# Kernel tuning notes

Hardware: AMD Instinct MI355X
Metric: run time of the kernel (lower is better)

The kernel has to match this reference:

```python
import jax, jax.numpy as jnp
import numpy as np
from jax import lax

T = 16        # in_length
E = 32        # input_embedding_size_d
H = 64        # encoder_size
NG = 32       # vehicles per scene group
G = 1024      # number of scene groups
N = G * NG    # total vehicles
C = 3         # class_num

leaky = lambda x: jax.nn.leaky_relu(x, 0.1)

def _gru_final(x_seq, Wih, Whh, bih, bhh):
    # x_seq: (T, N, E). PyTorch GRU gate order: r, z, n. Returns final hidden (N, H).
    def step(h, x):
        gx = x @ Wih.T + bih
        gh = h @ Whh.T + bhh
        xr, xz, xn = jnp.split(gx, 3, axis=-1)
        hr, hz, hn = jnp.split(gh, 3, axis=-1)
        r = jax.nn.sigmoid(xr + hr)
        z = jax.nn.sigmoid(xz + hz)
        ng = jnp.tanh(xn + r * hn)
        return (1.0 - z) * ng + z * h, None
    h0 = jnp.zeros((x_seq.shape[1], Whh.shape[1]), x_seq.dtype)
    hT, _ = lax.scan(step, h0, x_seq)
    return hT

def setup_inputs() -> dict:
    key = jax.random.key(0)
    ks = jax.random.split(key, 24)
    def rn(k, shape, fan):
        return jax.random.normal(k, shape, jnp.float32) * np.float32(1.0 / np.sqrt(fan))
    inp = {}
    inp["scene"] = jax.random.normal(ks[0], (N, 2 * T), jnp.float32)
    inp["condition"] = jax.random.randint(ks[1], (N,), 0, C, jnp.int32)
    inp["hero_pos_index"] = jax.random.randint(ks[2], (G,), 0, N, jnp.int32)
    inp["nbrs_pos_index"] = jax.random.randint(ks[3], (N,), 0, N, jnp.int32)
    inp["index_div"] = jnp.arange(N, dtype=jnp.int32).reshape(G, NG)
    # ip_emb_d: Linear(2, E)
    inp["W_emb"] = rn(ks[4], (2, E), 2)
    inp["b_emb"] = jnp.zeros((E,), jnp.float32)
    # forward / backward GRUs (weight_ih: (3H,E), weight_hh: (3H,H))
    inp["Wih_f"] = rn(ks[5], (3 * H, E), E); inp["Whh_f"] = rn(ks[6], (3 * H, H), H)
    inp["bih_f"] = jnp.zeros((3 * H,), jnp.float32); inp["bhh_f"] = jnp.zeros((3 * H,), jnp.float32)
    inp["Wih_b"] = rn(ks[7], (3 * H, E), E); inp["Whh_b"] = rn(ks[8], (3 * H, H), H)
    inp["bih_b"] = jnp.zeros((3 * H,), jnp.float32); inp["bhh_b"] = jnp.zeros((3 * H,), jnp.float32)
    # mlp: Linear(H, H//2)
    inp["Wm"] = rn(ks[9], (H, H // 2), H); inp["bm"] = jnp.zeros((H // 2,), jnp.float32)
    # spatial_mlp: Linear(2T, H) -> Linear(H, H//2)
    inp["Ws1"] = rn(ks[10], (2 * T, H), 2 * T); inp["bs1"] = jnp.zeros((H,), jnp.float32)
    inp["Ws2"] = rn(ks[11], (H, H // 2), H); inp["bs2"] = jnp.zeros((H // 2,), jnp.float32)
    # op_d: Linear(H, H//4) -> Linear(H//4, C)
    inp["Wo1"] = rn(ks[12], (H, H // 4), H); inp["bo1"] = jnp.zeros((H // 4,), jnp.float32)
    inp["Wo2"] = rn(ks[13], (H // 4, C), H // 4); inp["bo2"] = jnp.zeros((C,), jnp.float32)
    return inp

def reference(scene, condition, hero_pos_index, nbrs_pos_index, index_div,
              W_emb, b_emb, Wih_f, Whh_f, bih_f, bhh_f, Wih_b, Whh_b, bih_b, bhh_b,
              Wm, bm, Ws1, bs1, Ws2, bs2, Wo1, bo1, Wo2, bo2):
    n_total = scene.shape[0]
    # scene.view(-1,2,T).permute(2,0,1) -> (T, N, 2)
    scene_t = scene.reshape(n_total, 2, T).transpose(2, 0, 1)
    emb = leaky(scene_t @ W_emb + b_emb)                 # (T, N, E)
    h_f = _gru_final(emb, Wih_f, Whh_f, bih_f, bhh_f)    # (N, H)
    h_b = _gru_final(emb[::-1], Wih_b, Whh_b, bih_b, bhh_b)
    seq_enc = leaky(((h_f + h_b) * 0.5) @ Wm + bm)       # (N, H//2)
    # pairwise relative features within each group: rel[g, j, i] = x_i - x_j
    feat_g = scene[index_div]                            # (G, n, 2T); row layout == permute(1,2,0).view(-1,2T)
    rel = feat_g[:, None, :, :] - feat_g[:, :, None, :]  # (G, n, n, 2T)
    enc = leaky(leaky(rel @ Ws1 + bs1) @ Ws2 + bs2)      # (G, n, n, H//2)
    # diagonal pairs (i==j) are dropped in the original; subtract mlp(0) then divide by n-1
    zero_enc = leaky(leaky(bs1) @ Ws2 + bs2)             # (H//2,)
    n_grp = index_div.shape[1]
    pooled = (enc.sum(axis=2) - zero_enc) / (n_grp - 1)  # (G, n, H//2)
    pooled = pooled.reshape(n_total, -1)                 # group-concat order == vehicle order (arange groups)
    full_enc = jnp.concatenate([seq_enc, pooled], axis=1)  # (N, H)
    x_logit = leaky(full_enc @ Wo1 + bo1) @ Wo2 + bo2      # (N, C)
    return x_logit, full_enc
```

## Files before the change

### kernel.cpp

```cpp
#include <hip/hip_runtime.h>
#include <hip/hip_bf16.h>

#define TT 16
#define EE 32
#define HH 64
#define NGRP 32
#define CC 3

typedef __attribute__((ext_vector_type(8))) short short8;
typedef __attribute__((ext_vector_type(4))) float floatx4;

#define MFMA16(a, b, c) __builtin_amdgcn_mfma_f32_16x16x32_bf16((a), (b), (c), 0, 0, 0)

#define RLN2 1.4426950408889634f

__device__ __forceinline__ float leakyf(float x) { return fmaxf(x, 0.1f * x); }
__device__ __forceinline__ short f2bf(float x) {
    unsigned u = __float_as_uint(x);
    return (short)((u + 0x7FFFu + ((u >> 16) & 1u)) >> 16);
}
__device__ __forceinline__ short f2bf_h(float x) {
    return (short)((__float_as_uint(x) + 0x8000u) >> 16);
}
__device__ __forceinline__ float bf2f(short s) {
    return __uint_as_float(((unsigned)(unsigned short)s) << 16);
}
__device__ __forceinline__ short8 ld8bfs(const float* __restrict__ p, float s) {
    const float4 a = *(const float4*)p;
    const float4 b = *(const float4*)(p + 4);
    short8 v;
    v[0] = f2bf(a.x * s); v[1] = f2bf(a.y * s); v[2] = f2bf(a.z * s); v[3] = f2bf(a.w * s);
    v[4] = f2bf(b.x * s); v[5] = f2bf(b.y * s); v[6] = f2bf(b.z * s); v[7] = f2bf(b.w * s);
    return v;
}

__global__ __launch_bounds__(512, 6) void fused_kernel(
    const float* __restrict__ scene, const int* __restrict__ index_div,
    const float* __restrict__ W_emb, const float* __restrict__ b_emb,
    const float* __restrict__ Wih_f, const float* __restrict__ Whh_f,
    const float* __restrict__ bih_f, const float* __restrict__ bhh_f,
    const float* __restrict__ Wih_b, const float* __restrict__ Whh_b,
    const float* __restrict__ bih_b, const float* __restrict__ bhh_b,
    const float* __restrict__ Wm, const float* __restrict__ bm,
    const float* __restrict__ Ws1, const float* __restrict__ bs1,
    const float* __restrict__ Ws2, const float* __restrict__ bs2,
    const float* __restrict__ Wo1, const float* __restrict__ bo1,
    const float* __restrict__ Wo2, const float* __restrict__ bo2,
    float* __restrict__ full_enc, float* __restrict__ out)
{
    __shared__ __align__(16) union SmemU {
        struct {
            short Xall[16 * 2 * 64 * 8];
            short Hf[2 * 2 * 2 * 64 * 8];
        } g;
        struct {
            float su[NGRP][68];
            float fe[NGRP][68];
            float swo1[1024];
            float szero[32];
            float sscene2[32][33];
        } s;
    } sm;

    const int g    = blockIdx.x;
    const int tid  = threadIdx.x;
    const int lane = tid & 63;
    const int w    = __builtin_amdgcn_readfirstlane(tid >> 6);
    const int dir  = w >> 2;
    const int wd   = w & 3;
    const int cc   = lane & 15;
    const int quad = lane >> 4;
    const int j    = wd * 16 + cc;
    const int ks_w = j >> 5;
    const int qa_w = (j >> 3) & 3;
    const int ii_w = j & 7;
    const int rlane = (lane & 48) | ((lane & 3) << 2) | ((lane >> 2) & 3);

    {
        float* sc0 = (float*)sm.g.Hf;
        #pragma unroll
        for (int rep = 0; rep < 2; ++rep) {
            const int idx = tid + rep * 512;
            const int v = idx >> 5, c = idx & 31;
            const int n = index_div[g * NGRP + v];
            sc0[c * 33 + v] = scene[n * 32 + c];
        }
    }

    const float* Wih = dir ? Wih_b : Wih_f;
    const float* Whh = dir ? Whh_b : Whh_f;
    const float* bih = dir ? bih_b : bih_f;
    const float* bhh = dir ? bhh_b : bhh_f;
    const int k0 = quad * 8;
    const float SRZ = -RLN2, SN = 2.0f * RLN2;
    const short8 Br0  = ld8bfs(Whh + (j      ) * 64 + k0,      SRZ);
    const short8 Br1  = ld8bfs(Whh + (j      ) * 64 + 32 + k0, SRZ);
    const short8 Br2  = ld8bfs(Wih + (j      ) * 32 + k0,      SRZ);
    const short8 Bz0  = ld8bfs(Whh + (j +  64) * 64 + k0,      SRZ);
    const short8 Bz1  = ld8bfs(Whh + (j +  64) * 64 + 32 + k0, SRZ);
    const short8 Bz2  = ld8bfs(Wih + (j +  64) * 32 + k0,      SRZ);
    const short8 Bhn0 = ld8bfs(Whh + (j + 128) * 64 + k0,      SN);
    const short8 Bhn1 = ld8bfs(Whh + (j + 128) * 64 + 32 + k0, SN);
    const short8 Bxn  = ld8bfs(Wih + (j + 128) * 32 + k0,      SN);
    const float vb_r  = SRZ * (bih[j] + bhh[j]);
    const float vb_z  = SRZ * (bih[j + 64] + bhh[j + 64]);
    const float vb_xn = SN * bih[j + 128];
    const float vb_hn = SN * bhh[j + 128];

    __syncthreads();

    {
        const float* sc0 = (const float*)sm.g.Hf;
        const int t   = tid >> 5;
        const int veh = tid & 31;
        const float xs = sc0[t * 33 + veh];
        const float ys = sc0[(16 + t) * 33 + veh];
        const int mt = veh >> 4;
        const int m  = veh & 15;
        #pragma unroll
        for (int q = 0; q < 4; ++q) {
            short8 v;
            #pragma unroll
            for (int i2 = 0; i2 < 8; ++i2) {
                const int e = q * 8 + i2;
                v[i2] = f2bf(leakyf(fmaf(xs, W_emb[e], fmaf(ys, W_emb[EE + e], b_emb[e]))));
            }
            *(short8*)&sm.g.Xall[(((t * 2 + mt) * 64) + q * 16 + m) * 8] = v;
        }
    }
    __syncthreads();
    {
        const short8 z8 = {0, 0, 0, 0, 0, 0, 0, 0};
        *(short8*)&sm.g.Hf[tid * 8] = z8;
    }

    float h_reg[8];
    #pragma unroll
    for (int i = 0; i < 8; ++i) h_reg[i] = 0.0f;

    const int hf_dir = dir * 2048;
    __syncthreads();

    #pragma unroll 1
    for (int s = 0; s < TT; ++s) {
        const int t  = dir ? (TT - 1 - s) : s;
        const short* HfD = &sm.g.Hf[hf_dir];
        #pragma unroll
        for (int mt = 0; mt < 2; ++mt) {
            const short8 Ah0 = *(const short8*)&HfD[((0 * 2 + mt) * 64 + rlane) * 8];
            const short8 Ah1 = *(const short8*)&HfD[((1 * 2 + mt) * 64 + rlane) * 8];
            const short8 Axx = *(const short8*)&sm.g.Xall[((t * 2 + mt) * 64 + lane) * 8];
            const floatx4 z4 = {0.f, 0.f, 0.f, 0.f};

            const floatx4 ar = MFMA16(Axx, Br2, MFMA16(Ah1, Br1, MFMA16(Ah0, Br0, z4)));
            float rr[4];
            #pragma unroll
            for (int r = 0; r < 4; ++r)
                rr[r] = __builtin_amdgcn_rcpf(1.0f + __builtin_amdgcn_exp2f(ar[r] + vb_r));
            __builtin_amdgcn_sched_barrier(0);

            const floatx4 ahn = MFMA16(Ah1, Bhn1, MFMA16(Ah0, Bhn0, z4));
            const floatx4 axn = MFMA16(Axx, Bxn, z4);
            float ng[4];
            #pragma unroll
            for (int r = 0; r < 4; ++r) {
                const float y = fmaf(rr[r], ahn[r] + vb_hn, axn[r] + vb_xn);
                ng[r] = fmaf(-2.0f,
                             __builtin_amdgcn_rcpf(__builtin_amdgcn_exp2f(y) + 1.0f),
                             1.0f);
            }
            __builtin_amdgcn_sched_barrier(0);

            const floatx4 az = MFMA16(Axx, Bz2, MFMA16(Ah1, Bz1, MFMA16(Ah0, Bz0, z4)));
            #pragma unroll
            for (int r = 0; r < 4; ++r) {
                const float zz = __builtin_amdgcn_rcpf(1.0f + __builtin_amdgcn_exp2f(az[r] + vb_z));
                const float h0 = h_reg[mt * 4 + r];
                h_reg[mt * 4 + r] = fmaf(zz, h0 - ng[r], ng[r]);
            }
        }
        __syncthreads();
        short* HfW = &sm.g.Hf[hf_dir];
        #pragma unroll
        for (int mt = 0; mt < 2; ++mt) {
            #pragma unroll
            for (int r = 0; r < 4; ++r) {
                const int slot = qa_w * 16 + r * 4 + quad;
                HfW[((ks_w * 2 + mt) * 64 + slot) * 8 + ii_w] = f2bf_h(h_reg[mt * 4 + r]);
            }
        }
        __syncthreads();
    }

    #pragma unroll
    for (int rep = 0; rep < 2; ++rep) {
        const int idx = tid + rep * 512;
        const int v = idx >> 5, c = idx & 31;
        const int n = index_div[g * NGRP + v];
        sm.s.sscene2[c][v] = scene[n * 32 + c];
    }
    __syncthreads();

    if (w < 4) {
        const int nt   = w >> 1;
        const int mt_e = w & 1;
        const int n_col = nt * 16 + cc;
        short8 Bm0, Bm1;
        #pragma unroll
        for (int i = 0; i < 8; ++i) {
            Bm0[i] = f2bf(Wm[(     quad * 8 + i) * 32 + n_col]);
            Bm1[i] = f2bf(Wm[(32 + quad * 8 + i) * 32 + n_col]);
        }
        short8 A0, A1;
        #pragma unroll
        for (int ks = 0; ks < 2; ++ks) {
            const short8 F = *(const short8*)&sm.g.Hf[0    + ((ks * 2 + mt_e) * 64 + rlane) * 8];
            const short8 B = *(const short8*)&sm.g.Hf[2048 + ((ks * 2 + mt_e) * 64 + rlane) * 8];
            #pragma unroll
            for (int i = 0; i < 8; ++i) {
                const short v = f2bf(0.5f * (bf2f(F[i]) + bf2f(B[i])));
                if (ks == 0) A0[i] = v; else A1[i] = v;
            }
        }
        const floatx4 z4 = {0.f, 0.f, 0.f, 0.f};
        const floatx4 acc = MFMA16(A1, Bm1, MFMA16(A0, Bm0, z4));
        const float bmn = bm[n_col];
        #pragma unroll
        for (int r = 0; r < 4; ++r) {
            const int veh = mt_e * 16 + quad * 4 + r;
            const float sv = leakyf(acc[r] + bmn);
            const int n = index_div[g * NGRP + veh];
            full_enc[n * HH + n_col] = sv;
            sm.s.fe[veh][n_col] = sv;
        }
    } else {
        const int l  = tid & 255;
        const int v  = l >> 3;
        const int d0 = (l & 7) * 8;
        float acc[8];
        #pragma unroll
        for (int i = 0; i < 8; ++i) acc[i] = 0.0f;
        #pragma unroll
        for (int e = 0; e < EE; ++e) {
            const float f = sm.s.sscene2[e][v];
            const float4 w0 = *(const float4*)&Ws1[e * 64 + d0];
            const float4 w1 = *(const float4*)&Ws1[e * 64 + d0 + 4];
            acc[0] = fmaf(f, w0.x, acc[0]); acc[1] = fmaf(f, w0.y, acc[1]);
            acc[2] = fmaf(f, w0.z, acc[2]); acc[3] = fmaf(f, w0.w, acc[3]);
            acc[4] = fmaf(f, w1.x, acc[4]); acc[5] = fmaf(f, w1.y, acc[5]);
            acc[6] = fmaf(f, w1.z, acc[6]); acc[7] = fmaf(f, w1.w, acc[7]);
        }
        #pragma unroll
        for (int i = 0; i < 8; ++i) sm.s.su[v][d0 + i] = acc[i];
        *(float4*)&sm.s.swo1[l * 4] = *(const float4*)&Wo1[l * 4];
        if (l < 32) {
            float zs = bs2[l];
            #pragma unroll
            for (int d = 0; d < HH; ++d) zs = fmaf(leakyf(bs1[d]), Ws2[d * 32 + l], zs);
            sm.s.szero[l] = leakyf(zs);
        }
    }

    short8 Bw00, Bw01, Bw10, Bw11;
    #pragma unroll
    for (int i = 0; i < 8; ++i) {
        Bw00[i] = f2bf(Ws2[(     quad * 8 + i) * 32 + cc]);
        Bw01[i] = f2bf(Ws2[(32 + quad * 8 + i) * 32 + cc]);
        Bw10[i] = f2bf(Ws2[(     quad * 8 + i) * 32 + 16 + cc]);
        Bw11[i] = f2bf(Ws2[(32 + quad * 8 + i) * 32 + 16 + cc]);
    }
    float bsq0[8], bsq1[8];
    #pragma unroll
    for (int i = 0; i < 8; ++i) {
        bsq0[i] = bs1[quad * 8 + i];
        bsq1[i] = bs1[32 + quad * 8 + i];
    }
    const float bs2c0 = bs2[cc], bs2c1 = bs2[16 + cc];
    __syncthreads();

    #pragma unroll 2
    for (int jj = 0; jj < 4; ++jj) {
        const int jrow = w * 4 + jj;
        float vj0[8], vj1[8];
        #pragma unroll
        for (int i = 0; i < 8; ++i) {
            vj0[i] = sm.s.su[jrow][quad * 8 + i] - bsq0[i];
            vj1[i] = sm.s.su[jrow][32 + quad * 8 + i] - bsq1[i];
        }
        float acc0 = 0.0f, acc1 = 0.0f;
        #pragma unroll
        for (int it = 0; it < 2; ++it) {
            const int irow = it * 16 + cc;
            const float4 p0 = *(const float4*)&sm.s.su[irow][quad * 8];
            const float4 p1 = *(const float4*)&sm.s.su[irow][quad * 8 + 4];
            const float4 p2 = *(const float4*)&sm.s.su[irow][32 + quad * 8];
            const float4 p3 = *(const float4*)&sm.s.su[irow][32 + quad * 8 + 4];
            short8 A0, A1;
            A0[0] = f2bf(leakyf(p0.x - vj0[0])); A0[1] = f2bf(leakyf(p0.y - vj0[1]));
            A0[2] = f2bf(leakyf(p0.z - vj0[2])); A0[3] = f2bf(leakyf(p0.w - vj0[3]));
            A0[4] = f2bf(leakyf(p1.x - vj0[4])); A0[5] = f2bf(leakyf(p1.y - vj0[5]));
            A0[6] = f2bf(leakyf(p1.z - vj0[6])); A0[7] = f2bf(leakyf(p1.w - vj0[7]));
            A1[0] = f2bf(leakyf(p2.x - vj1[0])); A1[1] = f2bf(leakyf(p2.y - vj1[1]));
            A1[2] = f2bf(leakyf(p2.z - vj1[2])); A1[3] = f2bf(leakyf(p2.w - vj1[3]));
            A1[4] = f2bf(leakyf(p3.x - vj1[4])); A1[5] = f2bf(leakyf(p3.y - vj1[5]));
            A1[6] = f2bf(leakyf(p3.z - vj1[6])); A1[7] = f2bf(leakyf(p3.w - vj1[7]));
            const floatx4 z4 = {0.f, 0.f, 0.f, 0.f};
            const floatx4 D0 = MFMA16(A1, Bw01, MFMA16(A0, Bw00, z4));
            const floatx4 D1 = MFMA16(A1, Bw11, MFMA16(A0, Bw10, z4));
            #pragma unroll
            for (int r = 0; r < 4; ++r) {
                acc0 += leakyf(D0[r] + bs2c0);
                acc1 += leakyf(D1[r] + bs2c1);
            }
        }
        acc0 += __shfl_xor(acc0, 16, 64); acc0 += __shfl_xor(acc0, 32, 64);
        acc1 += __shfl_xor(acc1, 16, 64); acc1 += __shfl_xor(acc1, 32, 64);
        const int n = index_div[g * NGRP + jrow];
        if (quad == 0) {
            const float pv = (acc0 - sm.s.szero[cc]) * (1.0f / 31.0f);
            full_enc[n * HH + 32 + cc] = pv;
            sm.s.fe[jrow][32 + cc] = pv;
        } else if (quad == 1) {
            const float pv = (acc1 - sm.s.szero[16 + cc]) * (1.0f / 31.0f);
            full_enc[n * HH + 48 + cc] = pv;
            sm.s.fe[jrow][48 + cc] = pv;
        }
    }
    __syncthreads();

    {
        const int veh = tid >> 4;
        const int p   = tid & 15;
        float a = bo1[p];
        #pragma unroll
        for (int k = 0; k < HH; ++k)
            a = fmaf(sm.s.fe[veh][k], sm.s.swo1[k * 16 + p], a);
        a = leakyf(a);
        float l0 = a * Wo2[p * 3 + 0];
        float l1 = a * Wo2[p * 3 + 1];
        float l2 = a * Wo2[p * 3 + 2];
        #pragma unroll
        for (int off = 1; off < 16; off <<= 1) {
            l0 += __shfl_xor(l0, off, 64);
            l1 += __shfl_xor(l1, off, 64);
            l2 += __shfl_xor(l2, off, 64);
        }
        if (p == 0) {
            const int n = index_div[g * NGRP + veh];
            out[n * 3 + 0] = l0 + bo2[0];
            out[n * 3 + 1] = l1 + bo2[1];
            out[n * 3 + 2] = l2 + bo2[2];
        }
    }
}

extern "C" void kernel_launch(void* const* d_in, const int* in_sizes, int n_in,
                              void* d_out, int out_size, void* d_ws, size_t ws_size,
                              hipStream_t stream) {
    const float* scene     = (const float*)d_in[0];
    const int*   index_div = (const int*)d_in[4];
    const float* W_emb = (const float*)d_in[5];
    const float* b_emb = (const float*)d_in[6];
    const float* Wih_f = (const float*)d_in[7];
    const float* Whh_f = (const float*)d_in[8];
    const float* bih_f = (const float*)d_in[9];
    const float* bhh_f = (const float*)d_in[10];
    const float* Wih_b = (const float*)d_in[11];
    const float* Whh_b = (const float*)d_in[12];
    const float* bih_b = (const float*)d_in[13];
    const float* bhh_b = (const float*)d_in[14];
    const float* Wm  = (const float*)d_in[15];
    const float* bm  = (const float*)d_in[16];
    const float* Ws1 = (const float*)d_in[17];
    const float* bs1 = (const float*)d_in[18];
    const float* Ws2 = (const float*)d_in[19];
    const float* bs2 = (const float*)d_in[20];
    const float* Wo1 = (const float*)d_in[21];
    const float* bo1 = (const float*)d_in[22];
    const float* Wo2 = (const float*)d_in[23];
    const float* bo2 = (const float*)d_in[24];

    const int N = in_sizes[0] / (2 * TT);
    const int G = in_sizes[4] / NGRP;

    float* out      = (float*)d_out;
    float* full_enc = out + (size_t)N * CC;

    fused_kernel<<<dim3(G), dim3(512), 0, stream>>>(
        scene, index_div, W_emb, b_emb, Wih_f, Whh_f, bih_f, bhh_f,
        Wih_b, Whh_b, bih_b, bhh_b, Wm, bm, Ws1, bs1, Ws2, bs2,
        Wo1, bo1, Wo2, bo2, full_enc, out);
}
```

Measured before the change: 213.8 us.

## Pre-pack GRU weights to bf16 workspace and reload per step to cut registers

A one-block prep kernel converts and scales the GRU weight fragments to bf16 once and stores them in a workspace. The fused kernel stops holding all nine weight fragments in registers. It reloads them from the workspace inside each timestep, and the gate loops are restructured so the r, n and z phases each cover both row tiles. This lowers register pressure to improve occupancy or scheduling, at the cost of extra global/L2 loads per step and an additional kernel launch.

```diff
diff --git a/kernel.cpp b/kernel.cpp
--- a/kernel.cpp
+++ b/kernel.cpp
@@ -34,18 +34,49 @@
     return v;
 }
 
+__global__ __launch_bounds__(512) void prep_kernel(
+    const float* __restrict__ Wih_f, const float* __restrict__ Whh_f,
+    const float* __restrict__ Wih_b, const float* __restrict__ Whh_b,
+    short* __restrict__ wsf)
+{
+    const int tid  = threadIdx.x;
+    const int widx = tid >> 6;
+    const int lane = tid & 63;
+    const int dir  = widx >> 2;
+    const int wd   = widx & 3;
+    const int cc   = lane & 15;
+    const int quad = lane >> 4;
+    const int j    = wd * 16 + cc;
+    const int k0   = quad * 8;
+    const float* Wih = dir ? Wih_b : Wih_f;
+    const float* Whh = dir ? Whh_b : Whh_f;
+    const float SRZ = -RLN2, SN = 2.0f * RLN2;
+    short8 f[9];
+    f[0] = ld8bfs(Whh + (j      ) * 64 + k0,      SRZ);
+    f[1] = ld8bfs(Whh + (j      ) * 64 + 32 + k0, SRZ);
+    f[2] = ld8bfs(Wih + (j      ) * 32 + k0,      SRZ);
+    f[3] = ld8bfs(Whh + (j +  64) * 64 + k0,      SRZ);
+    f[4] = ld8bfs(Whh + (j +  64) * 64 + 32 + k0, SRZ);
+    f[5] = ld8bfs(Wih + (j +  64) * 32 + k0,      SRZ);
+    f[6] = ld8bfs(Whh + (j + 128) * 64 + k0,      SN);
+    f[7] = ld8bfs(Whh + (j + 128) * 64 + 32 + k0, SN);
+    f[8] = ld8bfs(Wih + (j + 128) * 32 + k0,      SN);
+    #pragma unroll
+    for (int fid = 0; fid < 9; ++fid)
+        *(short8*)&wsf[((widx * 9 + fid) * 64 + lane) * 8] = f[fid];
+}
+
 __global__ __launch_bounds__(512, 6) void fused_kernel(
     const float* __restrict__ scene, const int* __restrict__ index_div,
     const float* __restrict__ W_emb, const float* __restrict__ b_emb,
-    const float* __restrict__ Wih_f, const float* __restrict__ Whh_f,
     const float* __restrict__ bih_f, const float* __restrict__ bhh_f,
-    const float* __restrict__ Wih_b, const float* __restrict__ Whh_b,
     const float* __restrict__ bih_b, const float* __restrict__ bhh_b,
     const float* __restrict__ Wm, const float* __restrict__ bm,
     const float* __restrict__ Ws1, const float* __restrict__ bs1,
     const float* __restrict__ Ws2, const float* __restrict__ bs2,
     const float* __restrict__ Wo1, const float* __restrict__ bo1,
     const float* __restrict__ Wo2, const float* __restrict__ bo2,
+    const short* __restrict__ wsf,
     float* __restrict__ full_enc, float* __restrict__ out)
 {
     __shared__ __align__(16) union SmemU {
@@ -87,21 +118,9 @@
         }
     }
 
-    const float* Wih = dir ? Wih_b : Wih_f;
-    const float* Whh = dir ? Whh_b : Whh_f;
     const float* bih = dir ? bih_b : bih_f;
     const float* bhh = dir ? bhh_b : bhh_f;
-    const int k0 = quad * 8;
     const float SRZ = -RLN2, SN = 2.0f * RLN2;
-    const short8 Br0  = ld8bfs(Whh + (j      ) * 64 + k0,      SRZ);
-    const short8 Br1  = ld8bfs(Whh + (j      ) * 64 + 32 + k0, SRZ);
-    const short8 Br2  = ld8bfs(Wih + (j      ) * 32 + k0,      SRZ);
-    const short8 Bz0  = ld8bfs(Whh + (j +  64) * 64 + k0,      SRZ);
-    const short8 Bz1  = ld8bfs(Whh + (j +  64) * 64 + 32 + k0, SRZ);
-    const short8 Bz2  = ld8bfs(Wih + (j +  64) * 32 + k0,      SRZ);
-    const short8 Bhn0 = ld8bfs(Whh + (j + 128) * 64 + k0,      SN);
-    const short8 Bhn1 = ld8bfs(Whh + (j + 128) * 64 + 32 + k0, SN);
-    const short8 Bxn  = ld8bfs(Wih + (j + 128) * 32 + k0,      SN);
     const float vb_r  = SRZ * (bih[j] + bhh[j]);
     const float vb_z  = SRZ * (bih[j + 64] + bhh[j + 64]);
     const float vb_xn = SN * bih[j + 128];
@@ -141,44 +160,75 @@
     const int hf_dir = dir * 2048;
     __syncthreads();
 
+    const short* pB = wsf + ((size_t)(w * 9) * 64 + lane) * 8;
+    short8 BrA = *(const short8*)(pB + 0 * 512);
+    short8 BrB = *(const short8*)(pB + 1 * 512);
+    short8 BrC = *(const short8*)(pB + 2 * 512);
+    float rr[8], ng[8];
+
     #pragma unroll 1
     for (int s = 0; s < TT; ++s) {
+        asm("" : "+v"(pB));
+        const short8 Bn0 = *(const short8*)(pB + 6 * 512);
+        const short8 Bn1 = *(const short8*)(pB + 7 * 512);
+        const short8 Bn2 = *(const short8*)(pB + 8 * 512);
         const int t  = dir ? (TT - 1 - s) : s;
         const short* HfD = &sm.g.Hf[hf_dir];
+        const floatx4 z4 = {0.f, 0.f, 0.f, 0.f};
+
         #pragma unroll
         for (int mt = 0; mt < 2; ++mt) {
             const short8 Ah0 = *(const short8*)&HfD[((0 * 2 + mt) * 64 + rlane) * 8];
             const short8 Ah1 = *(const short8*)&HfD[((1 * 2 + mt) * 64 + rlane) * 8];
             const short8 Axx = *(const short8*)&sm.g.Xall[((t * 2 + mt) * 64 + lane) * 8];
-            const floatx4 z4 = {0.f, 0.f, 0.f, 0.f};
-
-            const floatx4 ar = MFMA16(Axx, Br2, MFMA16(Ah1, Br1, MFMA16(Ah0, Br0, z4)));
-            float rr[4];
+            const floatx4 ar = MFMA16(Axx, BrC, MFMA16(Ah1, BrB, MFMA16(Ah0, BrA, z4)));
             #pragma unroll
             for (int r = 0; r < 4; ++r)
-                rr[r] = __builtin_amdgcn_rcpf(1.0f + __builtin_amdgcn_exp2f(ar[r] + vb_r));
-            __builtin_amdgcn_sched_barrier(0);
-
-            const floatx4 ahn = MFMA16(Ah1, Bhn1, MFMA16(Ah0, Bhn0, z4));
-            const floatx4 axn = MFMA16(Axx, Bxn, z4);
-            float ng[4];
+                rr[mt * 4 + r] =
+                    __builtin_amdgcn_rcpf(1.0f + __builtin_amdgcn_exp2f(ar[r] + vb_r));
+        }
+        __builtin_amdgcn_sched_barrier(0);
+
+        #pragma unroll
+        for (int mt = 0; mt < 2; ++mt) {
+            const short8 Ah0 = *(const short8*)&HfD[((0 * 2 + mt) * 64 + rlane) * 8];
+            const short8 Ah1 = *(const short8*)&HfD[((1 * 2 + mt) * 64 + rlane) * 8];
+            const short8 Axx = *(const short8*)&sm.g.Xall[((t * 2 + mt) * 64 + lane) * 8];
+            const floatx4 ahn = MFMA16(Ah1, Bn1, MFMA16(Ah0, Bn0, z4));
+            const floatx4 axn = MFMA16(Axx, Bn2, z4);
             #pragma unroll
             for (int r = 0; r < 4; ++r) {
-                const float y = fmaf(rr[r], ahn[r] + vb_hn, axn[r] + vb_xn);
-                ng[r] = fmaf(-2.0f,
-                             __builtin_amdgcn_rcpf(__builtin_amdgcn_exp2f(y) + 1.0f),
-                             1.0f);
-            }
-            __builtin_amdgcn_sched_barrier(0);
-
-            const floatx4 az = MFMA16(Axx, Bz2, MFMA16(Ah1, Bz1, MFMA16(Ah0, Bz0, z4)));
-            #pragma unroll
-            for (int r = 0; r < 4; ++r) {
-                const float zz = __builtin_amdgcn_rcpf(1.0f + __builtin_amdgcn_exp2f(az[r] + vb_z));
-                const float h0 = h_reg[mt * 4 + r];
-                h_reg[mt * 4 + r] = fmaf(zz, h0 - ng[r], ng[r]);
-            }
-        }
+                const float y = fmaf(rr[mt * 4 + r], ahn[r] + vb_hn, axn[r] + vb_xn);
+                ng[mt * 4 + r] = fmaf(-2.0f,
+                                      __builtin_amdgcn_rcpf(__builtin_amdgcn_exp2f(y) + 1.0f),
+                                      1.0f);
+            }
+        }
+        __builtin_amdgcn_sched_barrier(0);
+
+        {
+            const short8 Bz0 = *(const short8*)(pB + 3 * 512);
+            const short8 Bz1 = *(const short8*)(pB + 4 * 512);
+            const short8 Bz2 = *(const short8*)(pB + 5 * 512);
+            #pragma unroll
+            for (int mt = 0; mt < 2; ++mt) {
+                const short8 Ah0 = *(const short8*)&HfD[((0 * 2 + mt) * 64 + rlane) * 8];
+                const short8 Ah1 = *(const short8*)&HfD[((1 * 2 + mt) * 64 + rlane) * 8];
+                const short8 Axx = *(const short8*)&sm.g.Xall[((t * 2 + mt) * 64 + lane) * 8];
+                const floatx4 az = MFMA16(Axx, Bz2, MFMA16(Ah1, Bz1, MFMA16(Ah0, Bz0, z4)));
+                #pragma unroll
+                for (int r = 0; r < 4; ++r) {
+                    const float zz =
+                        __builtin_amdgcn_rcpf(1.0f + __builtin_amdgcn_exp2f(az[r] + vb_z));
+                    const float h0 = h_reg[mt * 4 + r];
+                    h_reg[mt * 4 + r] = fmaf(zz, h0 - ng[mt * 4 + r], ng[mt * 4 + r]);
+                }
+            }
+        }
+        BrA = *(const short8*)(pB + 0 * 512);
+        BrB = *(const short8*)(pB + 1 * 512);
+        BrC = *(const short8*)(pB + 2 * 512);
+
         __syncthreads();
         short* HfW = &sm.g.Hf[hf_dir];
         #pragma unroll
@@ -385,9 +435,13 @@
 
     float* out      = (float*)d_out;
     float* full_enc = out + (size_t)N * CC;
+    short* wsf      = (short*)d_ws;
+
+    prep_kernel<<<dim3(1), dim3(512), 0, stream>>>(
+        Wih_f, Whh_f, Wih_b, Whh_b, wsf);
 
     fused_kernel<<<dim3(G), dim3(512), 0, stream>>>(
-        scene, index_div, W_emb, b_emb, Wih_f, Whh_f, bih_f, bhh_f,
-        Wih_b, Whh_b, bih_b, bhh_b, Wm, bm, Ws1, bs1, Ws2, bs2,
-        Wo1, bo1, Wo2, bo2, full_enc, out);
-}
+        scene, index_div, W_emb, b_emb, bih_f, bhh_f, bih_b, bhh_b,
+        Wm, bm, Ws1, bs1, Ws2, bs2, Wo1, bo1, Wo2, bo2, wsf,
+        full_enc, out);
+}
```

Measured after the change: 207.8 us. 2.8% less time.
